# Optimization experiments

Hardware: AMD Instinct MI355X
Metric: run time of the kernel (lower is better)

Reference implementation:

```python
import jax, jax.numpy as jnp
import numpy as np

B, T, D_IN, D_OUT, D_CTX, A_HID, L_CTX = 32, 256, 512, 512, 512, 512, 128


def setup_inputs() -> dict:
    key = jax.random.key(0)
    ks = jax.random.split(key, 10)
    s = 0.05  # small init scale to avoid gate saturation
    return {
        "x": jax.random.normal(ks[0], (B, T, D_IN), jnp.float32),
        "context": jax.random.normal(ks[1], (B, L_CTX, D_CTX), jnp.float32),
        "W": jax.random.normal(ks[2], (D_IN, 4 * D_OUT), jnp.float32) * s,
        "V": jax.random.normal(ks[3], (D_CTX, 4 * D_OUT), jnp.float32) * s,
        "U": jax.random.normal(ks[4], (D_OUT, 4 * D_OUT), jnp.float32) * s,
        "b": jnp.concatenate([
            jnp.zeros((D_OUT,), jnp.float32),        # b_i
            jnp.ones((D_OUT,), jnp.float32),         # b_f (forget bias init = ones)
            jnp.zeros((2 * D_OUT,), jnp.float32),    # b_c, b_o
        ]),
        "W_h_att": jax.random.normal(ks[5], (D_OUT, A_HID), jnp.float32) * s,
        "W_ctx_att": jax.random.normal(ks[6], (D_CTX, A_HID), jnp.float32) * s,
        "b_att": jnp.zeros((A_HID,), jnp.float32),
        "w_att_prj": jax.random.normal(ks[7], (A_HID, 1), jnp.float32) * s,
    }


def reference(x, context, W, V, U, b, W_h_att, W_ctx_att, b_att, w_att_prj):
    D = U.shape[0]  # output_dim
    # Precompute attention-projected context: (B, L, A)
    att_ctx = jnp.einsum("blc,ca->bla", context, W_ctx_att) + b_att
    # Precompute input contribution for all timesteps: (B, T, 4D)
    xW = jnp.einsum("btd,dk->btk", x, W)

    h0 = jnp.zeros((x.shape[0], D), x.dtype)
    c0 = jnp.zeros((x.shape[0], D), x.dtype)

    def step(carry, xw_t):
        h, c = carry
        # soft attention over context
        h_att = h @ W_h_att                                  # (B, A)
        preprj = jnp.tanh(h_att[:, None, :] + att_ctx)        # (B, L, A)
        prj = jnp.squeeze(preprj @ w_att_prj, -1)             # (B, L)
        alpha = jax.nn.softmax(prj, axis=-1)
        wctx = jnp.einsum("bl,blc->bc", alpha, context)       # (B, C)
        # LSTM gates; slice order follows the original step():
        # i=0, f=1, o=slice 2, candidate=slice 3
        preact = xw_t + wctx @ V + h @ U + b                  # (B, 4D)
        i = jax.nn.sigmoid(preact[:, :D])
        f = jax.nn.sigmoid(preact[:, D:2 * D])
        o = jax.nn.sigmoid(preact[:, 2 * D:3 * D])
        cand = jnp.tanh(preact[:, 3 * D:])
        c_new = f * c + i * cand
        h_new = o * jnp.tanh(c_new)
        return (h_new, c_new), h_new

    xw_seq = jnp.swapaxes(xW, 0, 1)                           # (T, B, 4D)
    _, hs = jax.lax.scan(step, (h0, c0), xw_seq)
    return jnp.swapaxes(hs, 0, 1)                             # (B, T, D)
```

## Files before the change

### kernel.cpp

```cpp
#include <hip/hip_runtime.h>
#include <hip/hip_fp16.h>

#define GD 256
#define BD 1024

constexpr int TSTEPS = 256;
constexpr int DD = 512;
constexpr int LC = 128;

constexpr size_t OFF_FLAGS_F = 0;
constexpr size_t OFF_REL_F   = 8192;
constexpr size_t OFF_GFLG_F  = 8448;
constexpr size_t OFF_SEXPP   = 16640;
constexpr size_t OFF_H16_F   = 49408;
constexpr size_t HO_HRING = 0;
constexpr size_t HO_ATT   = 4194304;
constexpr size_t HO_U16   = 6291456;
constexpr size_t HO_WH16  = 7340032;
constexpr size_t HO_CTXV  = 7602176;
constexpr size_t HO_XW    = 15990784;

typedef _Float16 h16;
typedef _Float16 h2  __attribute__((ext_vector_type(2)));
typedef _Float16 h8v __attribute__((ext_vector_type(8)));
union H8  { h8v v; h2 p[4]; };
union H2U { h2 h; unsigned u; };
union HSU { h16 h; unsigned short u; };

__device__ __forceinline__ float rcp_fast(float x) { return __builtin_amdgcn_rcpf(x); }
__device__ __forceinline__ float ftanh(float x) {
  float e = __expf(2.0f * x);
  return 1.0f - 2.0f * rcp_fast(e + 1.0f);
}
__device__ __forceinline__ float fsig(float x) { return rcp_fast(1.0f + __expf(-x)); }
__device__ __forceinline__ float fdot2(h2 a, h2 b, float c) {
  return __builtin_amdgcn_fdot2(a, b, c, false);
}

__device__ __forceinline__ float cloadf(const float* p) {
  return __hip_atomic_load(p, __ATOMIC_RELAXED, __HIP_MEMORY_SCOPE_AGENT);
}
__device__ __forceinline__ void cstoref(float* p, float v) {
  __hip_atomic_store(p, v, __ATOMIC_RELAXED, __HIP_MEMORY_SCOPE_AGENT);
}
__device__ __forceinline__ void cstoreu(unsigned* p, unsigned v) {
  __hip_atomic_store(p, v, __ATOMIC_RELAXED, __HIP_MEMORY_SCOPE_AGENT);
}
__device__ __forceinline__ void cstoreu8(unsigned long long* p, unsigned long long v) {
  __hip_atomic_store(p, v, __ATOMIC_RELAXED, __HIP_MEMORY_SCOPE_AGENT);
}
__device__ __forceinline__ void cstores(h16* p, h16 v) {
  HSU s; s.h = v;
  __hip_atomic_store((unsigned short*)p, s.u, __ATOMIC_RELAXED,
                     __HIP_MEMORY_SCOPE_AGENT);
}

__device__ __forceinline__ void gsync(int* flags, int* rel, int w, int& gen) {
  __syncthreads();
  gen++;
  const int t = threadIdx.x;
  if (w == 0) {
    if (t < 64) {
      if (t == 0)
        __hip_atomic_store(flags, gen, __ATOMIC_RELAXED, __HIP_MEMORY_SCOPE_AGENT);
      for (;;) {
        int m = gen;
#pragma unroll
        for (int i = 0; i < 4; i++) {
          int v = __hip_atomic_load(flags + (t + i * 64) * 32,
                                    __ATOMIC_RELAXED, __HIP_MEMORY_SCOPE_AGENT);
          m = (v < m) ? v : m;
        }
        if (__all(m >= gen)) break;
      }
      if (t == 0) {
#pragma unroll
        for (int i = 0; i < 8; i++)
          __hip_atomic_store(rel + i * 32, gen, __ATOMIC_RELAXED,
                             __HIP_MEMORY_SCOPE_AGENT);
      }
    }
    asm volatile("" ::: "memory");
  } else {
    if (t == 0) {
      __hip_atomic_store(flags + w * 32, gen, __ATOMIC_RELAXED,
                         __HIP_MEMORY_SCOPE_AGENT);
      const int* r = rel + (w & 7) * 32;
      while (__hip_atomic_load(r, __ATOMIC_RELAXED, __HIP_MEMORY_SCOPE_AGENT) < gen)
        __builtin_amdgcn_s_sleep(1);
    }
    asm volatile("" ::: "memory");
  }
  __syncthreads();
}

__device__ __forceinline__ void gbar(int* gf, int oct, int& sg) {
  __syncthreads();
  sg++;
  const int t = threadIdx.x;
  if (t < 64) {
    if (t == 0)
      __hip_atomic_store(gf + oct * 32, sg, __ATOMIC_RELAXED,
                         __HIP_MEMORY_SCOPE_AGENT);
    for (;;) {
      int v = sg;
      if (t < 8)
        v = __hip_atomic_load(gf + t * 32, __ATOMIC_RELAXED,
                              __HIP_MEMORY_SCOPE_AGENT);
      if (__all(v >= sg)) break;
      __builtin_amdgcn_s_sleep(1);
    }
  }
  asm volatile("" ::: "memory");
  __syncthreads();
}

__global__ __launch_bounds__(BD, 4) void attn_lstm_persistent(
    const float* __restrict__ x, const float* __restrict__ ctx,
    const float* __restrict__ W, const float* __restrict__ V,
    const float* __restrict__ U, const float* __restrict__ bias,
    const float* __restrict__ Wh, const float* __restrict__ Wc,
    const float* __restrict__ batt, const float* __restrict__ wprj,
    float* __restrict__ out, float* __restrict__ ws) {
  __shared__ __align__(16) unsigned char smem[58384];
  float* red    = (float*)(smem + 32768);
  float* hUk    = (float*)(smem + 49152);
  float* pre    = (float*)(smem + 50176);
  float* hattL  = (float*)(smem + 51200);
  float* sl     = (float*)(smem + 51456);
  float* spp    = (float*)(smem + 51968);
  float* biasS  = (float*)(smem + 56064);
  float* wprjL  = (float*)(smem + 57088);
  float* zinvS  = (float*)(smem + 57344);
  h2*    hLDS   = (h2*)(smem + 57360);

  const int w = blockIdx.x;
  const int t = threadIdx.x;
  const int b = w >> 3;
  const int oct = w & 7;

  int* flags = (int*)(ws + OFF_FLAGS_F);
  int* rel   = (int*)(ws + OFF_REL_F);
  int* gfl   = (int*)(ws + OFF_GFLG_F) + b * 256;
  float* sexpP = ws + OFF_SEXPP;
  h16* hb16   = (h16*)(ws + OFF_H16_F);
  h16* hringB = hb16 + HO_HRING;
  h16* att16  = hb16 + HO_ATT;
  h2*  U2     = (h2*)(hb16 + HO_U16) + (size_t)oct * 65536;
  h2*  Wh2    = (h2*)(hb16 + HO_WH16) + (size_t)oct * 16384;
  h16* ctxVp  = hb16 + HO_CTXV;
  h16* xw16   = hb16 + HO_XW;

  int gen = 0, sg = 0;
  float c_reg = 0.f;
  H8 pv0, pv1, pv2, pv3;

  {
    const int kp = w;
    {
      const float* r0p = U + (size_t)(2 * kp) * 2048;
      const float* r1p = r0p + 2048;
      const int col0 = 2 * t;
      float u00 = r0p[col0], u01 = r0p[col0 + 1];
      float u10 = r1p[col0], u11 = r1p[col0 + 1];
      int oc  = (col0 & 511) >> 6;
      int cc0 = ((col0 >> 9) << 6) | (col0 & 63);
      H2U p0; p0.h = h2{(h16)u00, (h16)u10};
      H2U p1; p1.h = h2{(h16)u01, (h16)u11};
      unsigned long long pk =
          (unsigned long long)p0.u | ((unsigned long long)p1.u << 32);
      cstoreu8((unsigned long long*)((h2*)(hb16 + HO_U16) +
                                     (size_t)oc * 65536 + (size_t)kp * 256 + cc0),
               pk);
    }
    if (t < 512) {
      float w0 = Wh[(size_t)(2 * kp) * DD + t];
      float w1 = Wh[(size_t)(2 * kp + 1) * DD + t];
      H2U pu; pu.h = h2{(h16)w0, (h16)w1};
      cstoreu((unsigned*)((h2*)(hb16 + HO_WH16) + (size_t)(t >> 6) * 16384 +
                          (size_t)kp * 64 + (t & 63)),
              pu.u);
    }
  }
  {
    float* fbuf = (float*)smem;
    const int r0 = w * 16;
#pragma unroll
    for (int i = 0; i < 2; i++) {
      int idx4 = i * BD + t;
      int row = idx4 >> 7, c4 = idx4 & 127;
      ((float4*)fbuf)[idx4] = ((const float4*)(ctx + (size_t)(r0 + row) * DD))[c4];
    }
    __syncthreads();
    const int a0 = t & 511, rh = t >> 9;
    float acc[8];
#pragma unroll
    for (int r = 0; r < 8; r++) acc[r] = 0.f;
    for (int cc = 0; cc < DD; cc++) {
      float wv = Wc[(size_t)cc * DD + a0];
#pragma unroll
      for (int r = 0; r < 8; r++)
        acc[r] += fbuf[(8 * rh + r) * DD + cc] * wv;
    }
    const float ba = batt[a0];
    for (int r = 0; r < 8; r++)
      cstores(att16 + (size_t)(r0 + 8 * rh + r) * DD + a0, (h16)(acc[r] + ba));
    __syncthreads();
  }
  if (t < 64) wprjL[t] = wprj[oct * 64 + t];
  if (t < 256) biasS[t] = bias[(size_t)(t >> 6) * 512 + 64 * oct + (t & 63)];

  {
    h2* xstage = (h2*)smem;
    for (int chk = 0; chk < 8; chk++) {
      const int st0 = chk * 32;
      {
        const int row = t >> 5, seg = t & 31;
        const float* src = x + ((size_t)b * TSTEPS + st0 + row) * DD + seg * 16;
        h2* dst = xstage + row * 256 + seg * 8;
#pragma unroll
        for (int q = 0; q < 4; q++) {
          float4 v = *(const float4*)(src + 4 * q);
          dst[2 * q]     = h2{(h16)v.x, (h16)v.y};
          dst[2 * q + 1] = h2{(h16)v.z, (h16)v.w};
        }
      }
      __syncthreads();
      const int cc = t & 255, sq = t >> 8;
      const int col = ((cc >> 6) << 9) + 64 * oct + (cc & 63);
      float acc[8];
#pragma unroll
      for (int j = 0; j < 8; j++) acc[j] = 0.f;
#pragma unroll 2
      for (int kp = 0; kp < 256; kp++) {
        float w0 = W[(size_t)(2 * kp) * 2048 + col];
        float w1 = W[(size_t)(2 * kp + 1) * 2048 + col];
        h2 wp = h2{(h16)w0, (h16)w1};
#pragma unroll
        for (int j = 0; j < 8; j++)
          acc[j] = fdot2(xstage[(sq * 8 + j) * 256 + kp], wp, acc[j]);
      }
#pragma unroll
      for (int j = 0; j < 8; j++)
        cstores(xw16 + (((size_t)(b * 8 + oct) * 256) + st0 + sq * 8 + j) * 256 + cc,
                (h16)acc[j]);
      __syncthreads();
    }
  }
  {
    h2* xstage = (h2*)smem;
    for (int chk = 0; chk < 4; chk++) {
      const int l0 = chk * 32;
      {
        const int row = t >> 5, seg = t & 31;
        const float* src = ctx + ((size_t)b * LC + l0 + row) * DD + seg * 16;
        h2* dst = xstage + row * 256 + seg * 8;
#pragma unroll
        for (int q = 0; q < 4; q++) {
          float4 v = *(const float4*)(src + 4 * q);
          dst[2 * q]     = h2{(h16)v.x, (h16)v.y};
          dst[2 * q + 1] = h2{(h16)v.z, (h16)v.w};
        }
      }
      __syncthreads();
      const int cc = t & 255, lq = t >> 8;
      const int col = ((cc >> 6) << 9) + 64 * oct + (cc & 63);
      float acc[8];
#pragma unroll
      for (int j = 0; j < 8; j++) acc[j] = 0.f;
#pragma unroll 2
      for (int kp = 0; kp < 256; kp++) {
        float v0 = V[(size_t)(2 * kp) * 2048 + col];
        float v1 = V[(size_t)(2 * kp + 1) * 2048 + col];
        h2 vp = h2{(h16)v0, (h16)v1};
#pragma unroll
        for (int j = 0; j < 8; j++)
          acc[j] = fdot2(xstage[(lq * 8 + j) * 256 + kp], vp, acc[j]);
      }
#pragma unroll
      for (int j = 0; j < 8; j++)
        cstores(ctxVp + (((size_t)(b * 8 + oct) * 128) + l0 + lq * 8 + j) * 256 + cc,
                (h16)acc[j]);
      __syncthreads();
    }
  }
  gsync(flags, rel, w, gen);

  {
    const int ccg = t & 31, lq = t >> 5;
    const h16* cvb = ctxVp + ((size_t)(b * 8 + oct) * 128) * 256 + ccg * 8;
    pv0.v = *(const h8v*)(cvb + (lq * 4 + 0) * 256);
    pv1.v = *(const h8v*)(cvb + (lq * 4 + 1) * 256);
    pv2.v = *(const h8v*)(cvb + (lq * 4 + 2) * 256);
    pv3.v = *(const h8v*)(cvb + (lq * 4 + 3) * 256);
  }

  for (int step = 0; step < TSTEPS; step++) {
    float xwv = 0.f;

    {
      if (t < 256) {
        unsigned hv = 0;
        if (step > 0)
          hv = *(const unsigned*)(hringB + ((size_t)b * TSTEPS + step - 1) * DD +
                                  2 * t);
        ((unsigned*)hLDS)[t] = hv;
      }
      __syncthreads();
      const int cc = t & 255, kq = t >> 8;
      const int kp0 = kq * 64;
      float f0 = 0.f, f1 = 0.f;
#pragma unroll 4
      for (int i = 0; i < 64; i += 2) {
        f0 = fdot2(hLDS[kp0 + i],     U2[(size_t)(kp0 + i) * 256 + cc],     f0);
        f1 = fdot2(hLDS[kp0 + i + 1], U2[(size_t)(kp0 + i + 1) * 256 + cc], f1);
      }
      red[kq * 256 + cc] = f0 + f1;
      if (t < 512) {
        const int a = t & 63, kg = t >> 6;
        const int kh0 = kg * 32;
        float ha = 0.f;
#pragma unroll 4
        for (int i = 0; i < 32; i++)
          ha = fdot2(hLDS[kh0 + i], Wh2[(size_t)(kh0 + i) * 64 + a], ha);
        red[1024 + kg * 64 + a] = ha;
      }
      if (t < 256)
        xwv = (float)xw16[(((size_t)(b * 8 + oct) * 256) + step) * 256 + t];
      __syncthreads();
      if (t < 256) {
        hUk[t] = red[t] + red[256 + t] + red[512 + t] + red[768 + t];
      } else if (t < 320) {
        int a = t - 256;
        float ha = 0.f;
#pragma unroll
        for (int kg = 0; kg < 8; kg++) ha += red[1024 + kg * 64 + a];
        hattL[a] = ha;
      }
      __syncthreads();
      {
        const int l = t >> 3, as = t & 7;
        H8 av;
        av.v = *(const h8v*)(att16 + (size_t)(b * LC + l) * DD + oct * 64 + as * 8);
        float p = 0.f;
#pragma unroll
        for (int j = 0; j < 8; j++)
          p += ftanh((float)av.v[j] + hattL[as * 8 + j]) * wprjL[as * 8 + j];
        p += __shfl_xor(p, 1); p += __shfl_xor(p, 2); p += __shfl_xor(p, 4);
        if (as == 0)
          cstoref(sexpP + ((size_t)b * 8 + oct) * 128 + l, p);
      }
    }
    gbar(gfl, oct, sg);

    {
      spp[t] = cloadf(sexpP + (size_t)b * 1024 + t);
      __syncthreads();
      if (t < 128) {
        float s = spp[t] + spp[128 + t] + spp[256 + t] + spp[384 + t] +
                  spp[512 + t] + spp[640 + t] + spp[768 + t] + spp[896 + t];
        sl[t] = __expf(s);
      }
      __syncthreads();
      if (t < 64) {
        float z = sl[t] + sl[t + 64];
        z += __shfl_xor(z, 32); z += __shfl_xor(z, 16); z += __shfl_xor(z, 8);
        z += __shfl_xor(z, 4);  z += __shfl_xor(z, 2);  z += __shfl_xor(z, 1);
        if (t == 0) *zinvS = rcp_fast(z);
      }
      const int ccg = t & 31, lq = t >> 5, w16 = t >> 6;
      float acc8[8];
#pragma unroll
      for (int j = 0; j < 8; j++) acc8[j] = 0.f;
      {
        float e0 = sl[lq * 4 + 0], e1 = sl[lq * 4 + 1];
        float e2 = sl[lq * 4 + 2], e3 = sl[lq * 4 + 3];
#pragma unroll
        for (int j = 0; j < 8; j++) {
          acc8[j] += e0 * (float)pv0.v[j];
          acc8[j] += e1 * (float)pv1.v[j];
          acc8[j] += e2 * (float)pv2.v[j];
          acc8[j] += e3 * (float)pv3.v[j];
        }
      }
#pragma unroll
      for (int j = 0; j < 8; j++) acc8[j] += __shfl_xor(acc8[j], 32);
      if ((t & 63) < 32) {
#pragma unroll
        for (int j = 0; j < 8; j++) red[w16 * 256 + ccg * 8 + j] = acc8[j];
      }
      __syncthreads();
      if (t < 256) {
        float pvs = 0.f;
#pragma unroll
        for (int k = 0; k < 16; k++) pvs += red[k * 256 + t];
        pre[t] = pvs * (*zinvS) + hUk[t] + xwv + biasS[t];
      }
      __syncthreads();
      if (t < 64) {
        const int d = t;
        float pi = pre[d], pf = pre[64 + d], po = pre[128 + d], pg = pre[192 + d];
        float ig = fsig(pi), fg = fsig(pf), og = fsig(po), gg = ftanh(pg);
        float cn = fg * c_reg + ig * gg;
        c_reg = cn;
        float hn = og * ftanh(cn);
        out[((size_t)b * TSTEPS + step) * DD + 64 * oct + d] = hn;
        cstores(hringB + ((size_t)b * TSTEPS + step) * DD + 64 * oct + d, (h16)hn);
      }
    }
    gbar(gfl, oct, sg);
  }
}

extern "C" void kernel_launch(void* const* d_in, const int* in_sizes, int n_in,
                              void* d_out, int out_size, void* d_ws, size_t ws_size,
                              hipStream_t stream) {
  (void)in_sizes; (void)n_in; (void)out_size; (void)ws_size;
  const float* x    = (const float*)d_in[0];
  const float* ctx  = (const float*)d_in[1];
  const float* W    = (const float*)d_in[2];
  const float* V    = (const float*)d_in[3];
  const float* U    = (const float*)d_in[4];
  const float* b    = (const float*)d_in[5];
  const float* Wh   = (const float*)d_in[6];
  const float* Wc   = (const float*)d_in[7];
  const float* batt = (const float*)d_in[8];
  const float* wprj = (const float*)d_in[9];

  hipMemsetAsync(d_ws, 0, (8192 + 256 + 8192) * sizeof(int), stream);

  hipLaunchKernelGGL(attn_lstm_persistent, dim3(GD), dim3(BD), 0, stream,
                     x, ctx, W, V, U, b, Wh, Wc, batt, wprj,
                     (float*)d_out, (float*)d_ws);
}
```

Baseline: 2.555 ms.

## Repartition recurrent work so each block handles 4 batches with register-resident weights

Work is split differently: each block now computes U and W_h slices for 4 batch rows, with the weight slices held in registers instead of being reread from global memory every step. Partial hU and attention scores go through global scratch, and barriers now span 32-block groups instead of 8. The context-V weights are packed as half2 for fdot2, and the softmax normalisation is applied before the weighted sum. This adds a wider barrier and an extra global exchange per step in return for less weight traffic per step.

Result: faster. 2.422 ms (-5.2%).

```diff
diff --git a/kernel.cpp b/kernel.cpp
--- a/kernel.cpp
+++ b/kernel.cpp
@@ -11,14 +11,15 @@
 constexpr size_t OFF_FLAGS_F = 0;
 constexpr size_t OFF_REL_F   = 8192;
 constexpr size_t OFF_GFLG_F  = 8448;
-constexpr size_t OFF_SEXPP   = 16640;
-constexpr size_t OFF_H16_F   = 49408;
-constexpr size_t HO_HRING = 0;
-constexpr size_t HO_ATT   = 4194304;
-constexpr size_t HO_U16   = 6291456;
-constexpr size_t HO_WH16  = 7340032;
-constexpr size_t HO_CTXV  = 7602176;
-constexpr size_t HO_XW    = 15990784;
+constexpr size_t OFF_HUX     = 16640;
+constexpr size_t OFF_SCP     = 82176;
+constexpr size_t OFF_H16_F   = 213248;
+constexpr size_t HO_HX    = 0;
+constexpr size_t HO_ATT   = 16384;
+constexpr size_t HO_U16   = 2113536;
+constexpr size_t HO_WH16  = 3162112;
+constexpr size_t HO_CTXV  = 3424256;
+constexpr size_t HO_XW    = 11812864;
 
 typedef _Float16 h16;
 typedef _Float16 h2  __attribute__((ext_vector_type(2)));
@@ -38,6 +39,9 @@
 }
 
 __device__ __forceinline__ float cloadf(const float* p) {
+  return __hip_atomic_load(p, __ATOMIC_RELAXED, __HIP_MEMORY_SCOPE_AGENT);
+}
+__device__ __forceinline__ unsigned cloadu(const unsigned* p) {
   return __hip_atomic_load(p, __ATOMIC_RELAXED, __HIP_MEMORY_SCOPE_AGENT);
 }
 __device__ __forceinline__ void cstoref(float* p, float v) {
@@ -94,17 +98,17 @@
   __syncthreads();
 }
 
-__device__ __forceinline__ void gbar(int* gf, int oct, int& sg) {
+__device__ __forceinline__ void gbar32(int* gf, int j, int& sg) {
   __syncthreads();
   sg++;
   const int t = threadIdx.x;
   if (t < 64) {
     if (t == 0)
-      __hip_atomic_store(gf + oct * 32, sg, __ATOMIC_RELAXED,
+      __hip_atomic_store(gf + j * 32, sg, __ATOMIC_RELAXED,
                          __HIP_MEMORY_SCOPE_AGENT);
     for (;;) {
       int v = sg;
-      if (t < 8)
+      if (t < 32)
         v = __hip_atomic_load(gf + t * 32, __ATOMIC_RELAXED,
                               __HIP_MEMORY_SCOPE_AGENT);
       if (__all(v >= sg)) break;
@@ -122,38 +126,40 @@
     const float* __restrict__ Wh, const float* __restrict__ Wc,
     const float* __restrict__ batt, const float* __restrict__ wprj,
     float* __restrict__ out, float* __restrict__ ws) {
-  __shared__ __align__(16) unsigned char smem[58384];
-  float* red    = (float*)(smem + 32768);
-  float* hUk    = (float*)(smem + 49152);
-  float* pre    = (float*)(smem + 50176);
-  float* hattL  = (float*)(smem + 51200);
-  float* sl     = (float*)(smem + 51456);
-  float* spp    = (float*)(smem + 51968);
-  float* biasS  = (float*)(smem + 56064);
-  float* wprjL  = (float*)(smem + 57088);
-  float* zinvS  = (float*)(smem + 57344);
-  h2*    hLDS   = (h2*)(smem + 57360);
+  __shared__ __align__(16) unsigned char smem[58448];
+  h16*   attcL = (h16*)smem;
+  float* red   = (float*)(smem + 18432);
+  float* red2  = (float*)(smem + 34816);
+  h2*    hLDS  = (h2*)(smem + 51200);
+  float* sl    = (float*)(smem + 55296);
+  h2*    anL   = (h2*)(smem + 55808);
+  float* hattL = (float*)(smem + 56064);
+  float* wpL   = (float*)(smem + 56320);
+  float* biasS = (float*)(smem + 56384);
+  float* pre   = (float*)(smem + 57408);
+  float* zinvS = (float*)(smem + 58432);
 
   const int w = blockIdx.x;
   const int t = threadIdx.x;
-  const int b = w >> 3;
-  const int oct = w & 7;
+  const int xg = w & 7;
+  const int j  = w >> 3;
+  const int q2 = j >> 3;
+  const int bb = 4 * xg + q2;
+  const int oct = j & 7;
 
   int* flags = (int*)(ws + OFF_FLAGS_F);
   int* rel   = (int*)(ws + OFF_REL_F);
-  int* gfl   = (int*)(ws + OFF_GFLG_F) + b * 256;
-  float* sexpP = ws + OFF_SEXPP;
-  h16* hb16   = (h16*)(ws + OFF_H16_F);
-  h16* hringB = hb16 + HO_HRING;
-  h16* att16  = hb16 + HO_ATT;
-  h2*  U2     = (h2*)(hb16 + HO_U16) + (size_t)oct * 65536;
-  h2*  Wh2    = (h2*)(hb16 + HO_WH16) + (size_t)oct * 16384;
-  h16* ctxVp  = hb16 + HO_CTXV;
-  h16* xw16   = hb16 + HO_XW;
+  int* gfl   = (int*)(ws + OFF_GFLG_F) + xg * 1024;
+  float* hUX = ws + OFF_HUX;
+  float* scP = ws + OFF_SCP;
+  h16* hb16  = (h16*)(ws + OFF_H16_F);
+  h16* hX    = hb16 + HO_HX;
+  h16* att16 = hb16 + HO_ATT;
+  h16* ctxVp = hb16 + HO_CTXV;
+  h16* xw16  = hb16 + HO_XW;
 
   int gen = 0, sg = 0;
   float c_reg = 0.f;
-  H8 pv0, pv1, pv2, pv3;
 
   {
     const int kp = w;
@@ -207,16 +213,14 @@
       cstores(att16 + (size_t)(r0 + 8 * rh + r) * DD + a0, (h16)(acc[r] + ba));
     __syncthreads();
   }
-  if (t < 64) wprjL[t] = wprj[oct * 64 + t];
-  if (t < 256) biasS[t] = bias[(size_t)(t >> 6) * 512 + 64 * oct + (t & 63)];
-
-  {
+  {
+    const int bS = w >> 3, octS = w & 7;
     h2* xstage = (h2*)smem;
     for (int chk = 0; chk < 8; chk++) {
       const int st0 = chk * 32;
       {
         const int row = t >> 5, seg = t & 31;
-        const float* src = x + ((size_t)b * TSTEPS + st0 + row) * DD + seg * 16;
+        const float* src = x + ((size_t)bS * TSTEPS + st0 + row) * DD + seg * 16;
         h2* dst = xstage + row * 256 + seg * 8;
 #pragma unroll
         for (int q = 0; q < 4; q++) {
@@ -227,33 +231,30 @@
       }
       __syncthreads();
       const int cc = t & 255, sq = t >> 8;
-      const int col = ((cc >> 6) << 9) + 64 * oct + (cc & 63);
+      const int col = ((cc >> 6) << 9) + 64 * octS + (cc & 63);
       float acc[8];
 #pragma unroll
-      for (int j = 0; j < 8; j++) acc[j] = 0.f;
+      for (int jj = 0; jj < 8; jj++) acc[jj] = 0.f;
 #pragma unroll 2
       for (int kp = 0; kp < 256; kp++) {
         float w0 = W[(size_t)(2 * kp) * 2048 + col];
         float w1 = W[(size_t)(2 * kp + 1) * 2048 + col];
         h2 wp = h2{(h16)w0, (h16)w1};
 #pragma unroll
-        for (int j = 0; j < 8; j++)
-          acc[j] = fdot2(xstage[(sq * 8 + j) * 256 + kp], wp, acc[j]);
-      }
-#pragma unroll
-      for (int j = 0; j < 8; j++)
-        cstores(xw16 + (((size_t)(b * 8 + oct) * 256) + st0 + sq * 8 + j) * 256 + cc,
-                (h16)acc[j]);
-      __syncthreads();
-    }
-  }
-  {
-    h2* xstage = (h2*)smem;
+        for (int jj = 0; jj < 8; jj++)
+          acc[jj] = fdot2(xstage[(sq * 8 + jj) * 256 + kp], wp, acc[jj]);
+      }
+#pragma unroll
+      for (int jj = 0; jj < 8; jj++)
+        cstores(xw16 + (((size_t)(bS * 8 + octS) * 256) + st0 + sq * 8 + jj) * 256 + cc,
+                (h16)acc[jj]);
+      __syncthreads();
+    }
     for (int chk = 0; chk < 4; chk++) {
       const int l0 = chk * 32;
       {
         const int row = t >> 5, seg = t & 31;
-        const float* src = ctx + ((size_t)b * LC + l0 + row) * DD + seg * 16;
+        const float* src = ctx + ((size_t)bS * LC + l0 + row) * DD + seg * 16;
         h2* dst = xstage + row * 256 + seg * 8;
 #pragma unroll
         for (int q = 0; q < 4; q++) {
@@ -264,101 +265,151 @@
       }
       __syncthreads();
       const int cc = t & 255, lq = t >> 8;
-      const int col = ((cc >> 6) << 9) + 64 * oct + (cc & 63);
+      const int col = ((cc >> 6) << 9) + 64 * octS + (cc & 63);
       float acc[8];
 #pragma unroll
-      for (int j = 0; j < 8; j++) acc[j] = 0.f;
+      for (int jj = 0; jj < 8; jj++) acc[jj] = 0.f;
 #pragma unroll 2
       for (int kp = 0; kp < 256; kp++) {
         float v0 = V[(size_t)(2 * kp) * 2048 + col];
         float v1 = V[(size_t)(2 * kp + 1) * 2048 + col];
         h2 vp = h2{(h16)v0, (h16)v1};
 #pragma unroll
-        for (int j = 0; j < 8; j++)
-          acc[j] = fdot2(xstage[(lq * 8 + j) * 256 + kp], vp, acc[j]);
-      }
-#pragma unroll
-      for (int j = 0; j < 8; j++)
-        cstores(ctxVp + (((size_t)(b * 8 + oct) * 128) + l0 + lq * 8 + j) * 256 + cc,
-                (h16)acc[j]);
+        for (int jj = 0; jj < 8; jj++)
+          acc[jj] = fdot2(xstage[(lq * 8 + jj) * 256 + kp], vp, acc[jj]);
+      }
+#pragma unroll
+      for (int jj = 0; jj < 8; jj++)
+        cstores(ctxVp + (((size_t)(bS * 8 + octS) * 128) + l0 + lq * 8 + jj) * 256 + cc,
+                (h16)acc[jj]);
       __syncthreads();
     }
   }
   gsync(flags, rel, w, gen);
 
+  const int ccL = t & 63, kseg = t >> 6;
+  const int aL = t & 15, ks2 = t >> 4;
+  h2 u[16], wh[4], cvp01[8], cvp23[8];
+  {
+    const h2* Ub = (const h2*)(hb16 + HO_U16) + (size_t)(j & 7) * 65536 +
+                   (size_t)(j >> 3) * 64 + ccL;
+#pragma unroll
+    for (int i = 0; i < 16; i++) u[i] = Ub[(size_t)(16 * kseg + i) * 256];
+    const h2* Wb = (const h2*)(hb16 + HO_WH16) + (size_t)(j >> 2) * 16384 +
+                   16 * (j & 3) + aL;
+#pragma unroll
+    for (int i = 0; i < 4; i++) wh[i] = Wb[(size_t)(4 * ks2 + i) * 64];
+  }
   {
     const int ccg = t & 31, lq = t >> 5;
-    const h16* cvb = ctxVp + ((size_t)(b * 8 + oct) * 128) * 256 + ccg * 8;
-    pv0.v = *(const h8v*)(cvb + (lq * 4 + 0) * 256);
-    pv1.v = *(const h8v*)(cvb + (lq * 4 + 1) * 256);
-    pv2.v = *(const h8v*)(cvb + (lq * 4 + 2) * 256);
-    pv3.v = *(const h8v*)(cvb + (lq * 4 + 3) * 256);
-  }
+    const h16* cvb = ctxVp + ((size_t)(bb * 8 + oct) * 128) * 256 + ccg * 8;
+    H8 p0, p1, p2, p3;
+    p0.v = *(const h8v*)(cvb + (size_t)(4 * lq + 0) * 256);
+    p1.v = *(const h8v*)(cvb + (size_t)(4 * lq + 1) * 256);
+    p2.v = *(const h8v*)(cvb + (size_t)(4 * lq + 2) * 256);
+    p3.v = *(const h8v*)(cvb + (size_t)(4 * lq + 3) * 256);
+#pragma unroll
+    for (int j8 = 0; j8 < 8; j8++) {
+      cvp01[j8] = h2{p0.v[j8], p1.v[j8]};
+      cvp23[j8] = h2{p2.v[j8], p3.v[j8]};
+    }
+  }
+  {
+    const int row = t >> 1, half = t & 1, q = row >> 7, l = row & 127;
+    uint4 v = *(const uint4*)(att16 + (size_t)((4 * xg + q) * LC + l) * DD +
+                              16 * j + 8 * half);
+    unsigned* dp = (unsigned*)(attcL + row * 18 + 8 * half);
+    dp[0] = v.x; dp[1] = v.y; dp[2] = v.z; dp[3] = v.w;
+  }
+  if (t < 16) wpL[t] = wprj[16 * j + t];
+  if (t < 256) biasS[t] = bias[(size_t)(t >> 6) * 512 + 64 * oct + (t & 63)];
+  __syncthreads();
 
   for (int step = 0; step < TSTEPS; step++) {
-    float xwv = 0.f;
-
     {
+      unsigned hv = 0;
+      if (step > 0)
+        hv = cloadu((const unsigned*)(hX + (size_t)(4 * xg + (t >> 8)) * DD +
+                                      2 * (t & 255)));
+      ((unsigned*)hLDS)[t] = hv;
+      __syncthreads();
+      {
+        float f0 = 0.f, f1 = 0.f, f2 = 0.f, f3 = 0.f;
+        const int base = 16 * kseg;
+#pragma unroll
+        for (int i = 0; i < 16; i++) {
+          h2 uu = u[i];
+          f0 = fdot2(hLDS[base + i], uu, f0);
+          f1 = fdot2(hLDS[256 + base + i], uu, f1);
+          f2 = fdot2(hLDS[512 + base + i], uu, f2);
+          f3 = fdot2(hLDS[768 + base + i], uu, f3);
+        }
+        red[kseg * 256 + ccL]       = f0;
+        red[kseg * 256 + 64 + ccL]  = f1;
+        red[kseg * 256 + 128 + ccL] = f2;
+        red[kseg * 256 + 192 + ccL] = f3;
+      }
+      {
+        float g0 = 0.f, g1 = 0.f, g2 = 0.f, g3 = 0.f;
+        const int base = 4 * ks2;
+#pragma unroll
+        for (int i = 0; i < 4; i++) {
+          h2 ww = wh[i];
+          g0 = fdot2(hLDS[base + i], ww, g0);
+          g1 = fdot2(hLDS[256 + base + i], ww, g1);
+          g2 = fdot2(hLDS[512 + base + i], ww, g2);
+          g3 = fdot2(hLDS[768 + base + i], ww, g3);
+        }
+        red2[ks2 * 64 + aL]      = g0;
+        red2[ks2 * 64 + 16 + aL] = g1;
+        red2[ks2 * 64 + 32 + aL] = g2;
+        red2[ks2 * 64 + 48 + aL] = g3;
+      }
+      __syncthreads();
       if (t < 256) {
-        unsigned hv = 0;
-        if (step > 0)
-          hv = *(const unsigned*)(hringB + ((size_t)b * TSTEPS + step - 1) * DD +
-                                  2 * t);
-        ((unsigned*)hLDS)[t] = hv;
-      }
-      __syncthreads();
-      const int cc = t & 255, kq = t >> 8;
-      const int kp0 = kq * 64;
-      float f0 = 0.f, f1 = 0.f;
-#pragma unroll 4
-      for (int i = 0; i < 64; i += 2) {
-        f0 = fdot2(hLDS[kp0 + i],     U2[(size_t)(kp0 + i) * 256 + cc],     f0);
-        f1 = fdot2(hLDS[kp0 + i + 1], U2[(size_t)(kp0 + i + 1) * 256 + cc], f1);
-      }
-      red[kq * 256 + cc] = f0 + f1;
-      if (t < 512) {
-        const int a = t & 63, kg = t >> 6;
-        const int kh0 = kg * 32;
-        float ha = 0.f;
-#pragma unroll 4
-        for (int i = 0; i < 32; i++)
-          ha = fdot2(hLDS[kh0 + i], Wh2[(size_t)(kh0 + i) * 64 + a], ha);
-        red[1024 + kg * 64 + a] = ha;
-      }
-      if (t < 256)
-        xwv = (float)xw16[(((size_t)(b * 8 + oct) * 256) + step) * 256 + t];
-      __syncthreads();
+        float s = 0.f;
+#pragma unroll
+        for (int k = 0; k < 16; k++) s += red[k * 256 + t];
+        cstoref(hUX + (size_t)(4 * xg + (t >> 6)) * 2048 + 64 * j + (t & 63), s);
+      } else if (t < 320) {
+        const int r = t - 256;
+        float s = 0.f;
+#pragma unroll
+        for (int k = 0; k < 64; k++) s += red2[k * 64 + r];
+        hattL[r] = s;
+      }
+      __syncthreads();
+      {
+        const int row = t >> 1, half = t & 1, q = row >> 7;
+        const h16* arow = attcL + row * 18 + 8 * half;
+        const float* hb_ = hattL + q * 16 + 8 * half;
+        const float* wp_ = wpL + 8 * half;
+        float p = 0.f;
+#pragma unroll
+        for (int aa = 0; aa < 8; aa++)
+          p += ftanh((float)arow[aa] + hb_[aa]) * wp_[aa];
+        p += __shfl_xor(p, 1);
+        if (half == 0)
+          cstoref(scP + (size_t)(4 * xg + q) * 4096 + j * 128 + (row & 127), p);
+      }
+    }
+    gbar32(gfl, j, sg);
+
+    {
+      float hUv = 0.f, xwv = 0.f;
       if (t < 256) {
-        hUk[t] = red[t] + red[256 + t] + red[512 + t] + red[768 + t];
-      } else if (t < 320) {
-        int a = t - 256;
-        float ha = 0.f;
-#pragma unroll
-        for (int kg = 0; kg < 8; kg++) ha += red[1024 + kg * 64 + a];
-        hattL[a] = ha;
-      }
-      __syncthreads();
-      {
-        const int l = t >> 3, as = t & 7;
-        H8 av;
-        av.v = *(const h8v*)(att16 + (size_t)(b * LC + l) * DD + oct * 64 + as * 8);
-        float p = 0.f;
-#pragma unroll
-        for (int j = 0; j < 8; j++)
-          p += ftanh((float)av.v[j] + hattL[as * 8 + j]) * wprjL[as * 8 + j];
-        p += __shfl_xor(p, 1); p += __shfl_xor(p, 2); p += __shfl_xor(p, 4);
-        if (as == 0)
-          cstoref(sexpP + ((size_t)b * 8 + oct) * 128 + l, p);
-      }
-    }
-    gbar(gfl, oct, sg);
-
-    {
-      spp[t] = cloadf(sexpP + (size_t)b * 1024 + t);
+        hUv = cloadf(hUX + (size_t)bb * 2048 + (size_t)(t >> 6) * 512 +
+                     64 * oct + (t & 63));
+        xwv = (float)xw16[(((size_t)(bb * 8 + oct)) * 256 + step) * 256 + t];
+      }
+#pragma unroll
+      for (int r = 0; r < 4; r++)
+        red[r * 1024 + t] = cloadf(scP + (size_t)bb * 4096 + r * 1024 + t);
       __syncthreads();
       if (t < 128) {
-        float s = spp[t] + spp[128 + t] + spp[256 + t] + spp[384 + t] +
-                  spp[512 + t] + spp[640 + t] + spp[768 + t] + spp[896 + t];
+        float s = 0.f;
+#pragma unroll
+        for (int jj = 0; jj < 32; jj++) s += red[jj * 128 + t];
         sl[t] = __expf(s);
       }
       __syncthreads();
@@ -368,33 +419,33 @@
         z += __shfl_xor(z, 4);  z += __shfl_xor(z, 2);  z += __shfl_xor(z, 1);
         if (t == 0) *zinvS = rcp_fast(z);
       }
-      const int ccg = t & 31, lq = t >> 5, w16 = t >> 6;
-      float acc8[8];
-#pragma unroll
-      for (int j = 0; j < 8; j++) acc8[j] = 0.f;
-      {
-        float e0 = sl[lq * 4 + 0], e1 = sl[lq * 4 + 1];
-        float e2 = sl[lq * 4 + 2], e3 = sl[lq * 4 + 3];
-#pragma unroll
-        for (int j = 0; j < 8; j++) {
-          acc8[j] += e0 * (float)pv0.v[j];
-          acc8[j] += e1 * (float)pv1.v[j];
-          acc8[j] += e2 * (float)pv2.v[j];
-          acc8[j] += e3 * (float)pv3.v[j];
-        }
-      }
-#pragma unroll
-      for (int j = 0; j < 8; j++) acc8[j] += __shfl_xor(acc8[j], 32);
-      if ((t & 63) < 32) {
-#pragma unroll
-        for (int j = 0; j < 8; j++) red[w16 * 256 + ccg * 8 + j] = acc8[j];
+      __syncthreads();
+      if (t < 64) {
+        float zi = *zinvS;
+        anL[t] = h2{(h16)(sl[2 * t] * zi), (h16)(sl[2 * t + 1] * zi)};
+      }
+      __syncthreads();
+      {
+        const int ccg = t & 31, lq = t >> 5, w16 = t >> 6;
+        h2 a01 = anL[2 * lq], a23 = anL[2 * lq + 1];
+        float acc8[8];
+#pragma unroll
+        for (int j8 = 0; j8 < 8; j8++)
+          acc8[j8] = fdot2(a23, cvp23[j8], fdot2(a01, cvp01[j8], 0.f));
+#pragma unroll
+        for (int j8 = 0; j8 < 8; j8++) acc8[j8] += __shfl_xor(acc8[j8], 32);
+        if ((t & 63) < 32) {
+#pragma unroll
+          for (int j8 = 0; j8 < 8; j8++)
+            red[w16 * 256 + ccg * 8 + j8] = acc8[j8];
+        }
       }
       __syncthreads();
       if (t < 256) {
         float pvs = 0.f;
 #pragma unroll
         for (int k = 0; k < 16; k++) pvs += red[k * 256 + t];
-        pre[t] = pvs * (*zinvS) + hUk[t] + xwv + biasS[t];
+        pre[t] = pvs + hUv + xwv + biasS[t];
       }
       __syncthreads();
       if (t < 64) {
@@ -404,11 +455,11 @@
         float cn = fg * c_reg + ig * gg;
         c_reg = cn;
         float hn = og * ftanh(cn);
-        out[((size_t)b * TSTEPS + step) * DD + 64 * oct + d] = hn;
-        cstores(hringB + ((size_t)b * TSTEPS + step) * DD + 64 * oct + d, (h16)hn);
-      }
-    }
-    gbar(gfl, oct, sg);
+        out[((size_t)bb * TSTEPS + step) * DD + 64 * oct + d] = hn;
+        cstores(hX + (size_t)bb * DD + 64 * oct + d, (h16)hn);
+      }
+    }
+    gbar32(gfl, j, sg);
   }
 }
 
```
